# Performance work log

Measured on AMD Instinct MI355X. Metric: run time of the kernel, lower is better.

## Reference

```python
import jax, jax.numpy as jnp
import numpy as np

NUM_HEADS = 16
THETA = 1000.0


def apply_rope(x, positions, theta):
    """x: [B, H, S, d_k]; positions: [S] float. Interleaved-pair RoPE."""
    d = x.shape[-1]
    inv_freq = theta ** (-jnp.arange(0, d, 2, dtype=x.dtype) / d)  # [d/2]
    ang = positions[:, None] * inv_freq[None, :]                    # [S, d/2]
    cos, sin = jnp.cos(ang), jnp.sin(ang)
    x1, x2 = x[..., 0::2], x[..., 1::2]
    r1 = x1 * cos - x2 * sin
    r2 = x1 * sin + x2 * cos
    return jnp.stack([r1, r2], axis=-1).reshape(x.shape)


def setup_inputs() -> dict:
    key = jax.random.key(0)
    ks = jax.random.split(key, 5)
    B, S, D = 2, 2048, 1024
    scale = 1.0 / np.sqrt(D)
    return {
        "in_features": jax.random.normal(ks[0], (B, S, D), jnp.float32),
        "q_proj_weight": jax.random.normal(ks[1], (D, D), jnp.float32) * scale,
        "k_proj_weight": jax.random.normal(ks[2], (D, D), jnp.float32) * scale,
        "v_proj_weight": jax.random.normal(ks[3], (D, D), jnp.float32) * scale,
        "o_proj_weight": jax.random.normal(ks[4], (D, D), jnp.float32) * scale,
        "token_positions": jnp.arange(S, dtype=jnp.int32),
    }


def reference(in_features, q_proj_weight, k_proj_weight, v_proj_weight,
              o_proj_weight, token_positions):
    B, S, D = in_features.shape
    H = NUM_HEADS
    d_k = D // H

    # Original rearrange: '(d_k heads) d_model -> heads d_model d_k'
    # => first dim splits as [d_k, heads] (heads is the inner factor).
    def split_heads(w):
        return w.reshape(d_k, H, D).transpose(1, 2, 0)  # [H, D, d_k]

    Wq, Wk, Wv = split_heads(q_proj_weight), split_heads(k_proj_weight), split_heads(v_proj_weight)

    xq = jnp.einsum("bsd,hdk->bhsk", in_features, Wq)
    xk = jnp.einsum("bsd,hdk->bhsk", in_features, Wk)
    xv = jnp.einsum("bsd,hdk->bhsk", in_features, Wv)

    pos = token_positions.astype(in_features.dtype)
    xq = apply_rope(xq, pos, THETA)
    xk = apply_rope(xk, pos, THETA)

    scores = jnp.einsum("bhqk,bhmk->bhqm", xq, xk) / jnp.sqrt(
        jnp.asarray(d_k, in_features.dtype))
    causal_mask = jnp.triu(jnp.ones((S, S), bool), k=1)  # True above diagonal
    scores = jnp.where(causal_mask, -jnp.inf, scores)
    attn = jax.nn.softmax(scores, axis=-1)

    out = jnp.einsum("bhqm,bhmv->bhqv", attn, xv)        # [B, H, S, d_k]
    out = out.transpose(0, 2, 1, 3).reshape(B, S, D)     # (heads d_emb) concat
    return out @ o_proj_weight                            # [B, S, d_o]
```

## Files before the change

### kernel.cpp

```cpp
#include <hip/hip_runtime.h>

typedef unsigned short u16;
typedef unsigned int u32;
typedef __bf16 bf16x8 __attribute__((ext_vector_type(8)));
typedef float f32x4 __attribute__((ext_vector_type(4)));

#define SEQ 2048
#define DMODEL 1024
#define NH 16
#define DK 64
#define BATCH 2
#define MTOT (BATCH * SEQ)

__device__ __forceinline__ u16 f2b(float f) {
  u32 u = __float_as_uint(f);
  u += 0x7fffu + ((u >> 16) & 1u);
  return (u16)(u >> 16);
}

__device__ __forceinline__ void gload16(const void* g, void* l) {
  __builtin_amdgcn_global_load_lds((const __attribute__((address_space(1))) u32*)g,
                                   (__attribute__((address_space(3))) u32*)l, 16, 0, 0);
}

__global__ __launch_bounds__(256) void cvt_bf16(const float* __restrict__ in,
                                                u16* __restrict__ out, int n4) {
  int i = blockIdx.x * 256 + threadIdx.x;
  if (i < n4) {
    float4 v = ((const float4*)in)[i];
    uint2 o;
    o.x = (u32)f2b(v.x) | ((u32)f2b(v.y) << 16);
    o.y = (u32)f2b(v.z) | ((u32)f2b(v.w) << 16);
    ((uint2*)out)[i] = o;
  }
}

__global__ __launch_bounds__(256) void cvt_w3(const float* __restrict__ wq,
                                              const float* __restrict__ wk,
                                              const float* __restrict__ wv,
                                              u16* __restrict__ oq,
                                              u16* __restrict__ ok,
                                              u16* __restrict__ ov) {
  const int m = blockIdx.y;
  const float* in = (m == 0) ? wq : ((m == 1) ? wk : wv);
  u16* out = (m == 0) ? oq : ((m == 1) ? ok : ov);
  const int i = blockIdx.x * 256 + threadIdx.x;
  float4 v = ((const float4*)in)[i];
  uint2 o;
  o.x = (u32)f2b(v.x) | ((u32)f2b(v.y) << 16);
  o.y = (u32)f2b(v.z) | ((u32)f2b(v.w) << 16);
  ((uint2*)out)[i] = o;
}

__global__ __launch_bounds__(256) void rope_tab_k(const int* __restrict__ tokpos,
                                                  float2* __restrict__ tab) {
  const int i = blockIdx.x * 256 + threadIdx.x;
  const int s = i >> 5, Xi = i & 31;
  const float invf = powf(1000.0f, -(float)Xi / 32.0f);
  const float ang = (float)tokpos[s] * invf;
  float sn, cs;
  sincosf(ang, &sn, &cs);
  tab[i] = make_float2(cs, sn);
}

__global__ __launch_bounds__(256) void transpose_wo(const float* __restrict__ wo,
                                                    u16* __restrict__ wot) {
  __shared__ float tile[32][33];
  const int bx = blockIdx.x * 32;
  const int by = blockIdx.y * 32;
  const int tx = threadIdx.x & 31, ty = threadIdx.x >> 5;
  for (int j = ty; j < 32; j += 8)
    tile[j][tx] = wo[(size_t)(by + j) * DMODEL + bx + tx];
  __syncthreads();
  for (int j = ty; j < 32; j += 8)
    wot[(size_t)(bx + j) * DMODEL + by + tx] = f2b(tile[tx][j]);
}

__device__ __forceinline__ void qkv_core(const u16* __restrict__ A,
                                         const u16* __restrict__ Bt,
                                         int mbase, int nbase,
                                         u16* As, u16* Bs, f32x4 acc[4][4]) {
  const int t = threadIdx.x;
  const int lane = t & 63, w = t >> 6;
  const int wr = w >> 1, wc = w & 1;
  const int l15 = lane & 15, lg = lane >> 4;
  const int srow = t >> 3;
  const int sch = (t & 7) ^ (srow & 7);
  const int rsw = l15 & 7;
  const int ASZ = 128 * 64;
  const int NIT = DMODEL / 64;

  auto stage = [&](int bufsel, int kb) {
    u16* Ad = &As[bufsel * ASZ];
    u16* Bd = &Bs[bufsel * ASZ];
#pragma unroll
    for (int j = 0; j < 4; ++j)
      gload16(&A[(size_t)(mbase + srow + 32 * j) * DMODEL + kb + sch * 8],
              &Ad[j * 2048 + t * 8]);
#pragma unroll
    for (int j = 0; j < 4; ++j)
      gload16(&Bt[(size_t)(nbase + srow + 32 * j) * DMODEL + kb + sch * 8],
              &Bd[j * 2048 + t * 8]);
  };

  auto compute = [&](int bufsel) {
    const u16* Ac = &As[bufsel * ASZ];
    const u16* Bc = &Bs[bufsel * ASZ];
#pragma unroll
    for (int kk = 0; kk < 2; ++kk) {
      bf16x8 af[4], bfr[4];
#pragma unroll
      for (int mi = 0; mi < 4; ++mi) {
        const int row = wr * 64 + mi * 16 + l15;
        af[mi] = *(const bf16x8*)&Ac[row * 64 + (((kk * 4 + lg) ^ rsw) * 8)];
      }
#pragma unroll
      for (int ni = 0; ni < 4; ++ni) {
        const int row = wc * 64 + ni * 16 + l15;
        bfr[ni] = *(const bf16x8*)&Bc[row * 64 + (((kk * 4 + lg) ^ rsw) * 8)];
      }
#pragma unroll
      for (int mi = 0; mi < 4; ++mi)
#pragma unroll
        for (int ni = 0; ni < 4; ++ni)
          acc[mi][ni] =
              __builtin_amdgcn_mfma_f32_16x16x32_bf16(af[mi], bfr[ni], acc[mi][ni], 0, 0, 0);
    }
  };

  stage(0, 0);

  for (int it = 0; it < NIT - 1; ++it) {
    const int buf = it & 1;
    stage(buf ^ 1, (it + 1) * 64);
    __builtin_amdgcn_sched_barrier(0);
    asm volatile("s_waitcnt vmcnt(8)" ::: "memory");
    __builtin_amdgcn_sched_barrier(0);
    __builtin_amdgcn_s_barrier();
    __builtin_amdgcn_sched_barrier(0);
    compute(buf);
    __builtin_amdgcn_sched_barrier(0);
    __builtin_amdgcn_s_barrier();
  }
  asm volatile("s_waitcnt vmcnt(0)" ::: "memory");
  __builtin_amdgcn_sched_barrier(0);
  __builtin_amdgcn_s_barrier();
  __builtin_amdgcn_sched_barrier(0);
  compute((DMODEL / 64 - 1) & 1);
}

__global__ __launch_bounds__(256) void gemm_qkv(
    const u16* __restrict__ Xb, const u16* __restrict__ Wqb,
    const u16* __restrict__ Wkb, const u16* __restrict__ Wvb,
    u16* __restrict__ Qb, u16* __restrict__ Kb, u16* __restrict__ Vb,
    const float2* __restrict__ tab) {
  __shared__ __align__(16) u16 As[2 * 128 * 64];
  __shared__ __align__(16) u16 Bs[2 * 128 * 64];

  const int mat = blockIdx.y >> 3;
  const int nbase = (blockIdx.y & 7) * 128;
  const int mbase = blockIdx.x * 128;
  const u16* Bt = (mat == 0) ? Wqb : ((mat == 1) ? Wkb : Wvb);

  f32x4 acc[4][4];
#pragma unroll
  for (int mi = 0; mi < 4; ++mi)
#pragma unroll
    for (int ni = 0; ni < 4; ++ni) {
      f32x4 z = {0.f, 0.f, 0.f, 0.f};
      acc[mi][ni] = z;
    }

  qkv_core(Xb, Bt, mbase, nbase, As, Bs, acc);

  const int t = threadIdx.x;
  const int lane = t & 63, w = t >> 6;
  const int wr = w >> 1, wc = w & 1;
  const int l15 = lane & 15, lg = lane >> 4;

  if (mat == 2) {
#pragma unroll
    for (int mi = 0; mi < 4; ++mi) {
#pragma unroll
      for (int r = 0; r < 4; ++r) {
        const int row = mbase + wr * 64 + mi * 16 + lg * 4 + r;
        const int bi = row >> 11, s = row & (SEQ - 1);
#pragma unroll
        for (int ni = 0; ni < 4; ++ni) {
          const int c = nbase + wc * 64 + ni * 16 + l15;
          const int hh = c & 15, vd = c >> 4;
          Vb[((size_t)((bi * NH + hh) * DK + vd)) * SEQ + s] = f2b(acc[mi][ni][r]);
        }
      }
    }
  } else {
    u16* Ob = (mat == 0) ? Qb : Kb;
    const float qscale = (mat == 0) ? 0.125f * 1.44269504088896f : 1.0f;
#pragma unroll
    for (int ni = 0; ni < 4; ni += 2) {
      const int Xi = (nbase + wc * 64 + ni * 16) >> 5;
#pragma unroll
      for (int mi = 0; mi < 4; ++mi) {
#pragma unroll
        for (int r = 0; r < 4; ++r) {
          const int row = mbase + wr * 64 + mi * 16 + lg * 4 + r;
          const int bi = row >> 11, s = row & (SEQ - 1);
          const float2 ct = tab[(s << 5) + Xi];
          const float x1 = acc[mi][ni][r], x2 = acc[mi][ni + 1][r];
          const float r1 = (x1 * ct.x - x2 * ct.y) * qscale;
          const float r2 = (x1 * ct.y + x2 * ct.x) * qscale;
          const u32 pk = (u32)f2b(r1) | ((u32)f2b(r2) << 16);
          *(u32*)&Ob[((size_t)((bi * NH + l15) * SEQ + s) << 6) + (Xi << 1)] = pk;
        }
      }
    }
  }
}

__global__ __launch_bounds__(256) void flash_attn(
    const u16* __restrict__ Qg, const u16* __restrict__ Kg,
    const u16* __restrict__ VTg, u16* __restrict__ Ag) {
  __shared__ __align__(16) u16 Ks[2][64 * 64];
  __shared__ __align__(16) u16 Vs[2][64 * 64];
  __shared__ __align__(16) u16 Ps[4][16][72];

  const int id = blockIdx.y * 32 + blockIdx.x;
  const int within = id >> 3;
  const int bh = (id & 7) * 4 + (within & 3);
  const int qt = 31 - (within >> 2);
  const int b = bh >> 4, h = bh & 15;
  const int qbase = qt * 64;

  const size_t hoff = (size_t)bh * SEQ * DK;
  const u16* Qh = Qg + hoff;
  const u16* Kh = Kg + hoff;
  const u16* VTh = VTg + hoff;

  const int t = threadIdx.x;
  const int lane = t & 63, w = t >> 6;
  const int l15 = lane & 15, lg = lane >> 4;
  const int sw = l15 & 7;

  const int qrow = qbase + w * 16 + l15;
  const bf16x8 qf0 = *(const bf16x8*)&Qh[(size_t)qrow * DK + lg * 8];
  const bf16x8 qf1 = *(const bf16x8*)&Qh[(size_t)qrow * DK + 32 + lg * 8];

  f32x4 oaccT[4];
#pragma unroll
  for (int vf = 0; vf < 4; ++vf) {
    f32x4 z = {0.f, 0.f, 0.f, 0.f};
    oaccT[vf] = z;
  }
  float m_r = -1e30f, l_r = 0.0f;

  const int srow = t >> 3;
  const int sc = ((t & 7) ^ (srow & 7)) * 8;

  gload16(&Kh[(size_t)srow * DK + sc], &Ks[0][t * 8]);
  gload16(&Kh[(size_t)(srow + 32) * DK + sc], &Ks[0][2048 + t * 8]);
  gload16(&VTh[(size_t)srow * SEQ + sc], &Vs[0][t * 8]);
  gload16(&VTh[(size_t)(srow + 32) * SEQ + sc], &Vs[0][2048 + t * 8]);

  for (int kt = 0; kt <= qt; ++kt) {
    const int buf = kt & 1;
    __syncthreads();
    if (kt < qt) {
      const int kb = (kt + 1) * 64;
      gload16(&Kh[(size_t)(kb + srow) * DK + sc], &Ks[buf ^ 1][t * 8]);
      gload16(&Kh[(size_t)(kb + srow + 32) * DK + sc], &Ks[buf ^ 1][2048 + t * 8]);
      gload16(&VTh[(size_t)srow * SEQ + kb + sc], &Vs[buf ^ 1][t * 8]);
      gload16(&VTh[(size_t)(srow + 32) * SEQ + kb + sc], &Vs[buf ^ 1][2048 + t * 8]);
    }
    const int kvbase = kt * 64;

    f32x4 sT[4];
#pragma unroll
    for (int f = 0; f < 4; ++f) {
      const int row = f * 16 + l15;
      bf16x8 k0 = *(const bf16x8*)&Ks[buf][row * 64 + (lg ^ sw) * 8];
      bf16x8 k1 = *(const bf16x8*)&Ks[buf][row * 64 + ((4 + lg) ^ sw) * 8];
      f32x4 z = {0.f, 0.f, 0.f, 0.f};
      z = __builtin_amdgcn_mfma_f32_16x16x32_bf16(k0, qf0, z, 0, 0, 0);
      z = __builtin_amdgcn_mfma_f32_16x16x32_bf16(k1, qf1, z, 0, 0, 0);
      sT[f] = z;
    }

    if (kt == qt) {
#pragma unroll
      for (int f = 0; f < 4; ++f)
#pragma unroll
        for (int r = 0; r < 4; ++r) {
          const int kvc = kvbase + f * 16 + lg * 4 + r;
          if (kvc > qrow) sT[f][r] = -1e30f;
        }
    }

    f32x4 mv;
#pragma unroll
    for (int r = 0; r < 4; ++r)
      mv[r] = fmaxf(fmaxf(sT[0][r], sT[1][r]), fmaxf(sT[2][r], sT[3][r]));
    float mx = fmaxf(fmaxf(mv[0], mv[1]), fmaxf(mv[2], mv[3]));
    mx = fmaxf(mx, __shfl_xor(mx, 16));
    mx = fmaxf(mx, __shfl_xor(mx, 32));

    const float mn = fmaxf(m_r, mx);
    const float alpha = exp2f(m_r - mn);
    m_r = mn;
#pragma unroll
    for (int f = 0; f < 4; ++f)
#pragma unroll
      for (int r = 0; r < 4; ++r) sT[f][r] = exp2f(sT[f][r] - mn);

    f32x4 rv;
#pragma unroll
    for (int r = 0; r < 4; ++r) rv[r] = (sT[0][r] + sT[1][r]) + (sT[2][r] + sT[3][r]);
    float rs = (rv[0] + rv[1]) + (rv[2] + rv[3]);
    rs += __shfl_xor(rs, 16);
    rs += __shfl_xor(rs, 32);
    l_r = l_r * alpha + rs;

#pragma unroll
    for (int vf = 0; vf < 4; ++vf)
#pragma unroll
      for (int r = 0; r < 4; ++r) oaccT[vf][r] *= alpha;

#pragma unroll
    for (int f = 0; f < 4; ++f) {
      uint2 pkv;
      pkv.x = (u32)f2b(sT[f][0]) | ((u32)f2b(sT[f][1]) << 16);
      pkv.y = (u32)f2b(sT[f][2]) | ((u32)f2b(sT[f][3]) << 16);
      *(uint2*)&Ps[w][l15][f * 16 + lg * 4] = pkv;
    }

#pragma unroll
    for (int c = 0; c < 2; ++c) {
      const bf16x8 pb = *(const bf16x8*)&Ps[w][l15][c * 32 + lg * 8];
#pragma unroll
      for (int vf = 0; vf < 4; ++vf) {
        const bf16x8 va =
            *(const bf16x8*)&Vs[buf][(vf * 16 + l15) * 64 + ((c * 4 + lg) ^ sw) * 8];
        oaccT[vf] = __builtin_amdgcn_mfma_f32_16x16x32_bf16(va, pb, oaccT[vf], 0, 0, 0);
      }
    }
  }

  const float inv = 1.0f / l_r;
  const size_t base = ((size_t)(b * SEQ + qrow)) * DMODEL + h * DK;
#pragma unroll
  for (int vf = 0; vf < 4; ++vf) {
    uint2 ov;
    ov.x = (u32)f2b(oaccT[vf][0] * inv) | ((u32)f2b(oaccT[vf][1] * inv) << 16);
    ov.y = (u32)f2b(oaccT[vf][2] * inv) | ((u32)f2b(oaccT[vf][3] * inv) << 16);
    *(uint2*)&Ag[base + vf * 16 + lg * 4] = ov;
  }
}

__global__ __launch_bounds__(256) void gemm_out(const u16* __restrict__ Ab,
                                                const u16* __restrict__ Wotb,
                                                float* __restrict__ Co) {
  __shared__ __align__(16) u16 As[64 * 64];
  __shared__ __align__(16) u16 Bs[128 * 64];
  const int mbase = blockIdx.x * 64, nbase = blockIdx.y * 128;

  const int t = threadIdx.x;
  const int lane = t & 63, w = t >> 6;
  const int wr = w >> 1, wc = w & 1;
  const int l15 = lane & 15, lg = lane >> 4;
  const int srow = t >> 3;
  const int sch = (t & 7) ^ (srow & 7);
  const int rsw = l15 & 7;

  f32x4 acc[2][4];
#pragma unroll
  for (int mi = 0; mi < 2; ++mi)
#pragma unroll
    for (int ni = 0; ni < 4; ++ni) {
      f32x4 z = {0.f, 0.f, 0.f, 0.f};
      acc[mi][ni] = z;
    }

  for (int kb = 0; kb < DMODEL; kb += 64) {
    gload16(&Ab[(size_t)(mbase + srow) * DMODEL + kb + sch * 8], &As[t * 8]);
    gload16(&Ab[(size_t)(mbase + 32 + srow) * DMODEL + kb + sch * 8], &As[2048 + t * 8]);
#pragma unroll
    for (int j = 0; j < 4; ++j)
      gload16(&Wotb[(size_t)(nbase + srow + 32 * j) * DMODEL + kb + sch * 8],
              &Bs[j * 2048 + t * 8]);
    __syncthreads();
#pragma unroll
    for (int kk = 0; kk < 2; ++kk) {
      bf16x8 af[2], bfr[4];
#pragma unroll
      for (int mi = 0; mi < 2; ++mi) {
        const int row = wr * 32 + mi * 16 + l15;
        af[mi] = *(const bf16x8*)&As[row * 64 + (((kk * 4 + lg) ^ rsw) * 8)];
      }
#pragma unroll
      for (int ni = 0; ni < 4; ++ni) {
        const int row = wc * 64 + ni * 16 + l15;
        bfr[ni] = *(const bf16x8*)&Bs[row * 64 + (((kk * 4 + lg) ^ rsw) * 8)];
      }
#pragma unroll
      for (int mi = 0; mi < 2; ++mi)
#pragma unroll
        for (int ni = 0; ni < 4; ++ni)
          acc[mi][ni] =
              __builtin_amdgcn_mfma_f32_16x16x32_bf16(af[mi], bfr[ni], acc[mi][ni], 0, 0, 0);
    }
    __syncthreads();
  }

#pragma unroll
  for (int mi = 0; mi < 2; ++mi) {
#pragma unroll
    for (int r = 0; r < 4; ++r) {
      const int row = mbase + wr * 32 + mi * 16 + lg * 4 + r;
#pragma unroll
      for (int ni = 0; ni < 4; ++ni) {
        const int c = nbase + wc * 64 + ni * 16 + l15;
        Co[(size_t)row * DMODEL + c] = acc[mi][ni][r];
      }
    }
  }
}

extern "C" void kernel_launch(void* const* d_in, const int* in_sizes, int n_in,
                              void* d_out, int out_size, void* d_ws, size_t ws_size,
                              hipStream_t stream) {
  const float* X = (const float*)d_in[0];
  const float* Wq = (const float*)d_in[1];
  const float* Wk = (const float*)d_in[2];
  const float* Wv = (const float*)d_in[3];
  const float* Wo = (const float*)d_in[4];
  const int* tokpos = (const int*)d_in[5];
  float* out = (float*)d_out;

  u16* p = (u16*)d_ws;
  u16* Xb = p;   p += (size_t)MTOT * DMODEL;
  u16* Wqb = p;  p += (size_t)DMODEL * DMODEL;
  u16* Wkb = p;  p += (size_t)DMODEL * DMODEL;
  u16* Wvb = p;  p += (size_t)DMODEL * DMODEL;
  u16* Wotb = p; p += (size_t)DMODEL * DMODEL;
  u16* Qb = p;   p += (size_t)BATCH * NH * SEQ * DK;
  u16* Kb = p;   p += (size_t)BATCH * NH * SEQ * DK;
  u16* Vb = p;   p += (size_t)BATCH * NH * SEQ * DK;
  float2* tab = (float2*)(p + 512);
  u16* Ab = Xb;

  cvt_bf16<<<4096, 256, 0, stream>>>(X, Xb, (MTOT * DMODEL) / 4);
  cvt_w3<<<dim3(1024, 3), 256, 0, stream>>>(Wq, Wk, Wv, Wqb, Wkb, Wvb);
  transpose_wo<<<dim3(32, 32), 256, 0, stream>>>(Wo, Wotb);
  rope_tab_k<<<(SEQ * 32) / 256, 256, 0, stream>>>(tokpos, tab);

  gemm_qkv<<<dim3(32, 24), 256, 0, stream>>>(Xb, Wqb, Wkb, Wvb, Qb, Kb, Vb, tab);
  flash_attn<<<dim3(32, 32), 256, 0, stream>>>(Qb, Kb, Vb, Ab);
  gemm_out<<<dim3(64, 8), 256, 0, stream>>>(Ab, Wotb, out);
}
```

Baseline: 141.5 us.

## Use partial vmcnt waits and explicit barriers in attention KV double-buffer loop

Restructures the K/V double-buffer loop so the next tile's global-to-LDS loads are issued first. The loop then waits only until the current tile's loads finish (vmcnt(4)) before a raw s_barrier, instead of a full __syncthreads drain. This keeps prefetch traffic in flight during the compute. A trailing barrier protects the buffer that the next iteration will overwrite. It also raises wave priority around the MFMA blocks via s_setprio to encourage interleaving of matrix work across waves. The cost is an extra barrier per iteration.

```diff
diff --git a/kernel.cpp b/kernel.cpp
--- a/kernel.cpp
+++ b/kernel.cpp
@@ -256,24 +256,33 @@
   const int srow = t >> 3;
   const int sc = ((t & 7) ^ (srow & 7)) * 8;
 
-  gload16(&Kh[(size_t)srow * DK + sc], &Ks[0][t * 8]);
-  gload16(&Kh[(size_t)(srow + 32) * DK + sc], &Ks[0][2048 + t * 8]);
-  gload16(&VTh[(size_t)srow * SEQ + sc], &Vs[0][t * 8]);
-  gload16(&VTh[(size_t)(srow + 32) * SEQ + sc], &Vs[0][2048 + t * 8]);
+  auto stageKV = [&](int bufsel, int kb) {
+    gload16(&Kh[(size_t)(kb + srow) * DK + sc], &Ks[bufsel][t * 8]);
+    gload16(&Kh[(size_t)(kb + srow + 32) * DK + sc], &Ks[bufsel][2048 + t * 8]);
+    gload16(&VTh[(size_t)srow * SEQ + kb + sc], &Vs[bufsel][t * 8]);
+    gload16(&VTh[(size_t)(srow + 32) * SEQ + kb + sc], &Vs[bufsel][2048 + t * 8]);
+  };
+
+  stageKV(0, 0);
 
   for (int kt = 0; kt <= qt; ++kt) {
     const int buf = kt & 1;
-    __syncthreads();
     if (kt < qt) {
-      const int kb = (kt + 1) * 64;
-      gload16(&Kh[(size_t)(kb + srow) * DK + sc], &Ks[buf ^ 1][t * 8]);
-      gload16(&Kh[(size_t)(kb + srow + 32) * DK + sc], &Ks[buf ^ 1][2048 + t * 8]);
-      gload16(&VTh[(size_t)srow * SEQ + kb + sc], &Vs[buf ^ 1][t * 8]);
-      gload16(&VTh[(size_t)(srow + 32) * SEQ + kb + sc], &Vs[buf ^ 1][2048 + t * 8]);
-    }
+      stageKV(buf ^ 1, (kt + 1) * 64);
+      __builtin_amdgcn_sched_barrier(0);
+      asm volatile("s_waitcnt vmcnt(4)" ::: "memory");
+    } else {
+      __builtin_amdgcn_sched_barrier(0);
+      asm volatile("s_waitcnt vmcnt(0)" ::: "memory");
+    }
+    __builtin_amdgcn_sched_barrier(0);
+    __builtin_amdgcn_s_barrier();
+    __builtin_amdgcn_sched_barrier(0);
+
     const int kvbase = kt * 64;
 
     f32x4 sT[4];
+    __builtin_amdgcn_s_setprio(1);
 #pragma unroll
     for (int f = 0; f < 4; ++f) {
       const int row = f * 16 + l15;
@@ -284,6 +293,7 @@
       z = __builtin_amdgcn_mfma_f32_16x16x32_bf16(k1, qf1, z, 0, 0, 0);
       sT[f] = z;
     }
+    __builtin_amdgcn_s_setprio(0);
 
     if (kt == qt) {
 #pragma unroll
@@ -332,6 +342,7 @@
       *(uint2*)&Ps[w][l15][f * 16 + lg * 4] = pkv;
     }
 
+    __builtin_amdgcn_s_setprio(1);
 #pragma unroll
     for (int c = 0; c < 2; ++c) {
       const bf16x8 pb = *(const bf16x8*)&Ps[w][l15][c * 32 + lg * 8];
@@ -342,6 +353,10 @@
         oaccT[vf] = __builtin_amdgcn_mfma_f32_16x16x32_bf16(va, pb, oaccT[vf], 0, 0, 0);
       }
     }
+    __builtin_amdgcn_s_setprio(0);
+
+    __builtin_amdgcn_sched_barrier(0);
+    __builtin_amdgcn_s_barrier();
   }
 
   const float inv = 1.0f / l_r;
```

New measurement: 142.4 us. About the same (+0.6%).
